# Kernel optimization log

Hardware: AMD Instinct MI355X
Metric: run time of the kernel (lower is better)

Reference implementation:

```python
import jax, jax.numpy as jnp
import numpy as np

B, NQ, NK, D = 64, 1024, 1024, 128
MASK_VALUE = -1e6


def setup_inputs() -> dict:
    key = jax.random.key(0)
    kq, kk, kv, kl = jax.random.split(key, 4)
    queries = jax.random.normal(kq, (B, NQ, D), dtype=jnp.float32)
    keys = jax.random.normal(kk, (B, NK, D), dtype=jnp.float32)
    values = jax.random.normal(kv, (B, NK, D), dtype=jnp.float32)
    valid_lens = jax.random.randint(kl, (B,), 1, NK + 1, dtype=jnp.int32)
    return {"queries": queries, "keys": keys, "values": values, "valid_lens": valid_lens}


def reference(queries, keys, values, valid_lens):
    d = queries.shape[-1]
    # scores: [B, Nq, Nk]
    scores = jnp.einsum("bqd,bkd->bqk", queries, keys) / jnp.sqrt(jnp.float32(d))
    # valid_lens [B] -> mask over last (key) axis, same for every query row
    key_pos = jnp.arange(scores.shape[-1])  # [Nk]
    mask = key_pos[None, None, :] < valid_lens[:, None, None]  # [B,1,Nk] broadcast
    scores = jnp.where(mask, scores, jnp.float32(MASK_VALUE))
    attn = jax.nn.softmax(scores, axis=-1)
    # dropout p=0.0 (eval): identity
    return jnp.einsum("bqk,bkd->bqd", attn, values)
```

## Files before the change

kernel.cpp:

```cpp
#include <hip/hip_runtime.h>

typedef __bf16 bf16x8 __attribute__((ext_vector_type(8)));
typedef __bf16 bf16x2 __attribute__((ext_vector_type(2)));
typedef float f32x4 __attribute__((ext_vector_type(4)));
typedef int i32x4 __attribute__((ext_vector_type(4)));

namespace {
constexpr int kNQ = 1024;
constexpr int kNK = 1024;
constexpr int kD = 128;
constexpr int kBQ = 64;
constexpr int kBK = 32;
constexpr int kTileElems = 4096;
constexpr float kScaleLog2e = 0.12751742f;
}

__device__ __forceinline__ int packbf(float a, float b) {
    bf16x2 t; t[0] = (__bf16)a; t[1] = (__bf16)b;
    return __builtin_bit_cast(int, t);
}

__device__ __forceinline__ void async16(const __bf16* g, const __bf16* l) {
    __builtin_amdgcn_global_load_lds(
        (const __attribute__((address_space(1))) void*)g,
        (__attribute__((address_space(3))) void*)l, 16, 0, 0);
}

__global__ void repack(const float* __restrict__ K, const float* __restrict__ V,
                       const int* __restrict__ VL,
                       __bf16* __restrict__ Kimg, __bf16* __restrict__ Vimg,
                       int* __restrict__ perm) {
    const int blk = blockIdx.x;

    if (blk == 64 * 32) {
        const int t = threadIdx.x;
        if (t < 64) {
            const int v = VL[t];
            int rank = 0;
            for (int j = 0; j < 64; ++j) {
                const int vj = VL[j];
                rank += (vj > v) || (vj == v && j < t);
            }
            perm[rank] = t;
        }
        return;
    }

    const int b = blk >> 5, t = blk & 31;
    if (t * kBK >= VL[b]) return;
    const int tid = threadIdx.x;
    __shared__ float vbuf[32 * 132];

    const size_t tileofs = (size_t)(b * 32 + t) * kTileElems;

    #pragma unroll
    for (int it = 0; it < 2; ++it) {
        const int chunk = tid + it * 256;
        const int k = chunk >> 4;
        const int p = chunk & 15;
        const int c = p ^ (k & 15);
        const float* src = K + (((size_t)b * kNK + t * kBK + k) * kD + c * 8);
        const f32x4 x0 = *(const f32x4*)src;
        const f32x4 x1 = *(const f32x4*)(src + 4);
        bf16x8 h;
        #pragma unroll
        for (int j = 0; j < 4; ++j) { h[j] = (__bf16)x0[j]; h[4 + j] = (__bf16)x1[j]; }
        *(bf16x8*)(Kimg + tileofs + chunk * 8) = h;
    }

    {
        const int r = tid >> 3, col0 = (tid & 7) * 16;
        const float* src = V + (((size_t)b * kNK + t * kBK + r) * kD + col0);
        #pragma unroll
        for (int j = 0; j < 4; ++j) {
            const f32x4 x = *(const f32x4*)(src + j * 4);
            *(f32x4*)&vbuf[r * 132 + col0 + j * 4] = x;
        }
    }
    __syncthreads();
    #pragma unroll
    for (int it = 0; it < 2; ++it) {
        const int chunk = tid + it * 256;
        const int d = chunk >> 2;
        const int p = chunk & 3;
        const int q = p ^ ((d >> 1) & 3);
        bf16x8 h;
        #pragma unroll
        for (int j = 0; j < 8; ++j) h[j] = (__bf16)vbuf[(q * 8 + j) * 132 + d];
        *(bf16x8*)(Vimg + tileofs + chunk * 8) = h;
    }
}

__global__ __launch_bounds__(256, 4)
void fa_fwd(const float* __restrict__ Q, const int* __restrict__ VL,
            const int* __restrict__ perm, const __bf16* __restrict__ Kimg,
            const __bf16* __restrict__ Vimg, float* __restrict__ O)
{
    __shared__ __align__(16) __bf16 kls[2][kTileElems];
    __shared__ __align__(16) __bf16 vls[2][kTileElems];

    const int tid  = threadIdx.x;
    const int wave = tid >> 6;
    const int lane = tid & 63;
    const int quad = lane >> 4;
    const int c16  = lane & 15;

    const int i = blockIdx.x;
    const int g = i >> 8;
    const int j = i & 255;
    int rank;
    if      (g == 0) rank = j;
    else if (g == 1) rank = 511 - j;
    else if (g == 2) rank = 512 + j;
    else             rank = 1023 - j;

    const int b    = perm[rank >> 4];
    const int qblk = rank & 15;
    const int q0   = qblk * kBQ + wave * 16;

    const int valid  = VL[b];
    const int ntiles = (valid + kBK - 1) / kBK;
    const size_t bT  = (size_t)b * 32;

    bf16x8 qf[4];
    {
        const float* qp = Q + ((size_t)b * kNQ + q0 + c16) * kD + quad * 8;
        #pragma unroll
        for (int f = 0; f < 4; ++f) {
            const f32x4 x0 = *(const f32x4*)(qp + f * 32);
            const f32x4 x1 = *(const f32x4*)(qp + f * 32 + 4);
            #pragma unroll
            for (int jj = 0; jj < 4; ++jj) {
                qf[f][jj]     = (__bf16)x0[jj];
                qf[f][4 + jj] = (__bf16)x1[jj];
            }
        }
    }

    bf16x8 ones;
    #pragma unroll
    for (int jj = 0; jj < 8; ++jj) ones[jj] = (__bf16)1.0f;

    f32x4 acc[9];
    #pragma unroll
    for (int f = 0; f < 9; ++f) {
        acc[f][0] = 0.f; acc[f][1] = 0.f; acc[f][2] = 0.f; acc[f][3] = 0.f;
    }

    auto stage = [&](int bufi, int t) {
        const __bf16* kg = Kimg + (bT + t) * kTileElems;
        const __bf16* vg = Vimg + (bT + t) * kTileElems;
        #pragma unroll
        for (int ii = 0; ii < 2; ++ii) {
            const int seg = (wave * 2 + ii) * 512;
            async16(kg + seg + lane * 8, &kls[bufi][seg]);
            async16(vg + seg + lane * 8, &vls[bufi][seg]);
        }
    };

    const int a0 = ((quad & 1) << 7) + (c16 << 2);
    const int a1 = a0 + 64;
    const bool lo = quad < 2;

    const int vsw = (quad ^ ((c16 >> 1) & 3)) << 3;

    stage(0, 0);
    __syncthreads();

    for (int t = 0; t < ntiles; ++t) {
        const int cur = t & 1;
        if (t + 1 < ntiles) stage(cur ^ 1, t + 1);

        f32x4 s0a = {0.f,0.f,0.f,0.f}, s0b = {0.f,0.f,0.f,0.f};
        f32x4 s1a = {0.f,0.f,0.f,0.f}, s1b = {0.f,0.f,0.f,0.f};
        const __bf16* kbuf = kls[cur];
        #pragma unroll
        for (int f = 0; f < 2; ++f) {
            const bf16x8 kf = *(const bf16x8*)&kbuf[c16 * 128 + (((f * 4 + quad) ^ c16) << 3)];
            s0a = __builtin_amdgcn_mfma_f32_16x16x32_bf16(kf, qf[f], s0a, 0, 0, 0);
        }
        #pragma unroll
        for (int f = 2; f < 4; ++f) {
            const bf16x8 kf = *(const bf16x8*)&kbuf[c16 * 128 + (((f * 4 + quad) ^ c16) << 3)];
            s0b = __builtin_amdgcn_mfma_f32_16x16x32_bf16(kf, qf[f], s0b, 0, 0, 0);
        }
        #pragma unroll
        for (int f = 0; f < 2; ++f) {
            const bf16x8 kf = *(const bf16x8*)&kbuf[(16 + c16) * 128 + (((f * 4 + quad) ^ c16) << 3)];
            s1a = __builtin_amdgcn_mfma_f32_16x16x32_bf16(kf, qf[f], s1a, 0, 0, 0);
        }
        #pragma unroll
        for (int f = 2; f < 4; ++f) {
            const bf16x8 kf = *(const bf16x8*)&kbuf[(16 + c16) * 128 + (((f * 4 + quad) ^ c16) << 3)];
            s1b = __builtin_amdgcn_mfma_f32_16x16x32_bf16(kf, qf[f], s1b, 0, 0, 0);
        }
        f32x4 s0 = s0a + s0b;
        f32x4 s1 = s1a + s1b;

        const int kb = t * kBK;
        if (kb + kBK > valid) {
            #pragma unroll
            for (int r = 0; r < 4; ++r) {
                if (kb + quad * 4 + r >= valid)      s0[r] = -1e30f;
                if (kb + 16 + quad * 4 + r >= valid) s1[r] = -1e30f;
            }
        }

        #pragma unroll
        for (int r = 0; r < 4; ++r) {
            s0[r] = __builtin_amdgcn_exp2f(s0[r] * kScaleLog2e);
            s1[r] = __builtin_amdgcn_exp2f(s1[r] * kScaleLog2e);
        }

        const int pp01 = packbf(s0[0], s0[1]), pp23 = packbf(s0[2], s0[3]);
        const int qq01 = packbf(s1[0], s1[1]), qq23 = packbf(s1[2], s1[3]);
        const int b0p = __builtin_amdgcn_ds_bpermute(a0, pp01);
        const int b0q = __builtin_amdgcn_ds_bpermute(a0, qq01);
        const int b1p = __builtin_amdgcn_ds_bpermute(a0, pp23);
        const int b1q = __builtin_amdgcn_ds_bpermute(a0, qq23);
        const int b2p = __builtin_amdgcn_ds_bpermute(a1, pp01);
        const int b2q = __builtin_amdgcn_ds_bpermute(a1, qq01);
        const int b3p = __builtin_amdgcn_ds_bpermute(a1, pp23);
        const int b3q = __builtin_amdgcn_ds_bpermute(a1, qq23);
        i32x4 pd;
        pd[0] = lo ? b0p : b0q;
        pd[1] = lo ? b1p : b1q;
        pd[2] = lo ? b2p : b2q;
        pd[3] = lo ? b3p : b3q;
        const bf16x8 pf = __builtin_bit_cast(bf16x8, pd);

        const __bf16* vbuf = vls[cur];
        #pragma unroll
        for (int f = 0; f < 8; ++f) {
            const bf16x8 vf = *(const bf16x8*)&vbuf[(f * 16 + c16) * 32 + vsw];
            acc[f] = __builtin_amdgcn_mfma_f32_16x16x32_bf16(pf, vf, acc[f], 0, 0, 0);
        }
        acc[8] = __builtin_amdgcn_mfma_f32_16x16x32_bf16(pf, ones, acc[8], 0, 0, 0);

        __syncthreads();
    }

    float* ob = O + ((size_t)b * kNQ + q0) * kD;
    #pragma unroll
    for (int r = 0; r < 4; ++r) {
        const float inv = 1.0f / acc[8][r];
        #pragma unroll
        for (int f = 0; f < 8; ++f) {
            ob[(quad * 4 + r) * kD + f * 16 + c16] = acc[f][r] * inv;
        }
    }
}

extern "C" void kernel_launch(void* const* d_in, const int* in_sizes, int n_in,
                              void* d_out, int out_size, void* d_ws, size_t ws_size,
                              hipStream_t stream) {
    const float* Q = (const float*)d_in[0];
    const float* K = (const float*)d_in[1];
    const float* V = (const float*)d_in[2];
    const int*  VL = (const int*)d_in[3];
    float* O = (float*)d_out;

    int* perm = (int*)d_ws;
    __bf16* Kimg = (__bf16*)((char*)d_ws + 4096);
    __bf16* Vimg = (__bf16*)((char*)d_ws + 4096 + (size_t)16 * 1024 * 1024);

    repack<<<dim3(64 * 32 + 1), 256, 0, stream>>>(K, V, VL, Kimg, Vimg, perm);
    fa_fwd<<<dim3(1024), 256, 0, stream>>>(Q, VL, perm, Kimg, Vimg, O);
}
```

Measured before the change: 165.8 us.

## Load K tiles directly into registers in MFMA fragment order, bypassing LDS

The prep kernel now writes the bf16 K image in per-lane MFMA fragment order, so each wave loads its K fragments straight from global memory into registers with coalesced 16-byte loads instead of staging through LDS. The main loop is unrolled by two with ping-pong register buffers (kA/kB) that prefetch the next tile's K while V still goes through double-buffered LDS. This halves LDS traffic and LDS footprint, which could raise occupancy. In exchange it adds 16 bf16x8 register fragments per thread, and each of the four waves re-reads the same K tile from global memory or L2.

```diff
diff --git a/kernel.cpp b/kernel.cpp
--- a/kernel.cpp
+++ b/kernel.cpp
@@ -55,17 +55,20 @@
 
     #pragma unroll
     for (int it = 0; it < 2; ++it) {
-        const int chunk = tid + it * 256;
-        const int k = chunk >> 4;
-        const int p = chunk & 15;
-        const int c = p ^ (k & 15);
-        const float* src = K + (((size_t)b * kNK + t * kBK + k) * kD + c * 8);
+        const int ch = tid + it * 256;
+        const int s  = ch >> 8;
+        const int f  = (ch >> 6) & 3;
+        const int qd = (ch >> 4) & 3;
+        const int c  = ch & 15;
+        const int key = s * 16 + c;
+        const int dch = f * 4 + qd;
+        const float* src = K + (((size_t)b * kNK + t * kBK + key) * kD + dch * 8);
         const f32x4 x0 = *(const f32x4*)src;
         const f32x4 x1 = *(const f32x4*)(src + 4);
         bf16x8 h;
         #pragma unroll
         for (int j = 0; j < 4; ++j) { h[j] = (__bf16)x0[j]; h[4 + j] = (__bf16)x1[j]; }
-        *(bf16x8*)(Kimg + tileofs + chunk * 8) = h;
+        *(bf16x8*)(Kimg + tileofs + ch * 8) = h;
     }
 
     {
@@ -96,7 +99,6 @@
             const int* __restrict__ perm, const __bf16* __restrict__ Kimg,
             const __bf16* __restrict__ Vimg, float* __restrict__ O)
 {
-    __shared__ __align__(16) __bf16 kls[2][kTileElems];
     __shared__ __align__(16) __bf16 vls[2][kTileElems];
 
     const int tid  = threadIdx.x;
@@ -122,6 +124,26 @@
     const int ntiles = (valid + kBK - 1) / kBK;
     const size_t bT  = (size_t)b * 32;
 
+    auto stage = [&](int bufi, int t) {
+        const __bf16* vg = Vimg + (bT + t) * kTileElems;
+        #pragma unroll
+        for (int ii = 0; ii < 2; ++ii) {
+            const int seg = (wave * 2 + ii) * 512;
+            async16(vg + seg + lane * 8, &vls[bufi][seg]);
+        }
+    };
+
+    bf16x8 kA[8], kB[8];
+#define LOADK(dst, tt) do {                                              \
+        const __bf16* kg_ = Kimg + (bT + (tt)) * kTileElems;             \
+        _Pragma("unroll")                                                \
+        for (int u = 0; u < 8; ++u)                                      \
+            dst[u] = *(const bf16x8*)(kg_ + u * 512 + lane * 8);         \
+    } while (0)
+
+    LOADK(kA, 0);
+    stage(0, 0);
+
     bf16x8 qf[4];
     {
         const float* qp = Q + ((size_t)b * kNQ + q0 + c16) * kD + quad * 8;
@@ -147,53 +169,23 @@
         acc[f][0] = 0.f; acc[f][1] = 0.f; acc[f][2] = 0.f; acc[f][3] = 0.f;
     }
 
-    auto stage = [&](int bufi, int t) {
-        const __bf16* kg = Kimg + (bT + t) * kTileElems;
-        const __bf16* vg = Vimg + (bT + t) * kTileElems;
-        #pragma unroll
-        for (int ii = 0; ii < 2; ++ii) {
-            const int seg = (wave * 2 + ii) * 512;
-            async16(kg + seg + lane * 8, &kls[bufi][seg]);
-            async16(vg + seg + lane * 8, &vls[bufi][seg]);
-        }
-    };
-
     const int a0 = ((quad & 1) << 7) + (c16 << 2);
     const int a1 = a0 + 64;
     const bool lo = quad < 2;
 
     const int vsw = (quad ^ ((c16 >> 1) & 3)) << 3;
 
-    stage(0, 0);
-    __syncthreads();
-
-    for (int t = 0; t < ntiles; ++t) {
-        const int cur = t & 1;
-        if (t + 1 < ntiles) stage(cur ^ 1, t + 1);
-
+    auto computeTile = [&](const bf16x8 (&kfr)[8], const __bf16* vbuf, int t) {
         f32x4 s0a = {0.f,0.f,0.f,0.f}, s0b = {0.f,0.f,0.f,0.f};
         f32x4 s1a = {0.f,0.f,0.f,0.f}, s1b = {0.f,0.f,0.f,0.f};
-        const __bf16* kbuf = kls[cur];
-        #pragma unroll
-        for (int f = 0; f < 2; ++f) {
-            const bf16x8 kf = *(const bf16x8*)&kbuf[c16 * 128 + (((f * 4 + quad) ^ c16) << 3)];
-            s0a = __builtin_amdgcn_mfma_f32_16x16x32_bf16(kf, qf[f], s0a, 0, 0, 0);
-        }
-        #pragma unroll
-        for (int f = 2; f < 4; ++f) {
-            const bf16x8 kf = *(const bf16x8*)&kbuf[c16 * 128 + (((f * 4 + quad) ^ c16) << 3)];
-            s0b = __builtin_amdgcn_mfma_f32_16x16x32_bf16(kf, qf[f], s0b, 0, 0, 0);
-        }
-        #pragma unroll
-        for (int f = 0; f < 2; ++f) {
-            const bf16x8 kf = *(const bf16x8*)&kbuf[(16 + c16) * 128 + (((f * 4 + quad) ^ c16) << 3)];
-            s1a = __builtin_amdgcn_mfma_f32_16x16x32_bf16(kf, qf[f], s1a, 0, 0, 0);
-        }
-        #pragma unroll
-        for (int f = 2; f < 4; ++f) {
-            const bf16x8 kf = *(const bf16x8*)&kbuf[(16 + c16) * 128 + (((f * 4 + quad) ^ c16) << 3)];
-            s1b = __builtin_amdgcn_mfma_f32_16x16x32_bf16(kf, qf[f], s1b, 0, 0, 0);
-        }
+        s0a = __builtin_amdgcn_mfma_f32_16x16x32_bf16(kfr[0], qf[0], s0a, 0, 0, 0);
+        s0a = __builtin_amdgcn_mfma_f32_16x16x32_bf16(kfr[1], qf[1], s0a, 0, 0, 0);
+        s0b = __builtin_amdgcn_mfma_f32_16x16x32_bf16(kfr[2], qf[2], s0b, 0, 0, 0);
+        s0b = __builtin_amdgcn_mfma_f32_16x16x32_bf16(kfr[3], qf[3], s0b, 0, 0, 0);
+        s1a = __builtin_amdgcn_mfma_f32_16x16x32_bf16(kfr[4], qf[0], s1a, 0, 0, 0);
+        s1a = __builtin_amdgcn_mfma_f32_16x16x32_bf16(kfr[5], qf[1], s1a, 0, 0, 0);
+        s1b = __builtin_amdgcn_mfma_f32_16x16x32_bf16(kfr[6], qf[2], s1b, 0, 0, 0);
+        s1b = __builtin_amdgcn_mfma_f32_16x16x32_bf16(kfr[7], qf[3], s1b, 0, 0, 0);
         f32x4 s0 = s0a + s0b;
         f32x4 s1 = s1a + s1b;
 
@@ -229,16 +221,32 @@
         pd[3] = lo ? b3p : b3q;
         const bf16x8 pf = __builtin_bit_cast(bf16x8, pd);
 
-        const __bf16* vbuf = vls[cur];
         #pragma unroll
         for (int f = 0; f < 8; ++f) {
             const bf16x8 vf = *(const bf16x8*)&vbuf[(f * 16 + c16) * 32 + vsw];
             acc[f] = __builtin_amdgcn_mfma_f32_16x16x32_bf16(pf, vf, acc[f], 0, 0, 0);
         }
         acc[8] = __builtin_amdgcn_mfma_f32_16x16x32_bf16(pf, ones, acc[8], 0, 0, 0);
-
+    };
+
+    __syncthreads();
+
+    int t = 0;
+    while (true) {
+        const bool more1 = (t + 1 < ntiles);
+        if (more1) { LOADK(kB, t + 1); stage(1, t + 1); }
+        computeTile(kA, vls[0], t);
         __syncthreads();
-    }
+        if (!more1) break;
+
+        const bool more2 = (t + 2 < ntiles);
+        if (more2) { LOADK(kA, t + 2); stage(0, t + 2); }
+        computeTile(kB, vls[1], t + 1);
+        __syncthreads();
+        if (!more2) break;
+        t += 2;
+    }
+#undef LOADK
 
     float* ob = O + ((size_t)b * kNQ + q0) * kD;
     #pragma unroll
```

Result: slower. 265.1 us (+59.9%).

## Use 512-thread blocks with 4-slot LDS ring and prefetch depth two

Applied to the files above, without the earlier changes.

Doubles the query rows per block to 128 (8 waves) so each staged K/V tile is shared by twice as many waves, halving K/V LDS traffic per query. It replaces the double buffer plus end-of-iteration __syncthreads with a 4-slot ring prefetched two tiles ahead, gated by explicit vmcnt waits and a single s_barrier. It also raises wave priority around the MFMA sections. The cost is more LDS per block (64 KB), fewer blocks to balance across CUs under variable valid lengths, and reliance on hand-written vmcnt counts being correct.

```diff
diff --git a/kernel.cpp b/kernel.cpp
--- a/kernel.cpp
+++ b/kernel.cpp
@@ -9,7 +9,6 @@
 constexpr int kNQ = 1024;
 constexpr int kNK = 1024;
 constexpr int kD = 128;
-constexpr int kBQ = 64;
 constexpr int kBK = 32;
 constexpr int kTileElems = 4096;
 constexpr float kScaleLog2e = 0.12751742f;
@@ -91,13 +90,13 @@
     }
 }
 
-__global__ __launch_bounds__(256, 4)
+__global__ __launch_bounds__(512, 4)
 void fa_fwd(const float* __restrict__ Q, const int* __restrict__ VL,
             const int* __restrict__ perm, const __bf16* __restrict__ Kimg,
             const __bf16* __restrict__ Vimg, float* __restrict__ O)
 {
-    __shared__ __align__(16) __bf16 kls[2][kTileElems];
-    __shared__ __align__(16) __bf16 vls[2][kTileElems];
+    __shared__ __align__(16) __bf16 kls[4][kTileElems];
+    __shared__ __align__(16) __bf16 vls[4][kTileElems];
 
     const int tid  = threadIdx.x;
     const int wave = tid >> 6;
@@ -106,21 +105,26 @@
     const int c16  = lane & 15;
 
     const int i = blockIdx.x;
-    const int g = i >> 8;
     const int j = i & 255;
-    int rank;
-    if      (g == 0) rank = j;
-    else if (g == 1) rank = 511 - j;
-    else if (g == 2) rank = 512 + j;
-    else             rank = 1023 - j;
-
-    const int b    = perm[rank >> 4];
-    const int qblk = rank & 15;
-    const int q0   = qblk * kBQ + wave * 16;
+    const int rank = (i >> 8) ? (511 - j) : j;
+
+    const int b  = perm[rank >> 3];
+    const int q0 = (rank & 7) * 128 + wave * 16;
 
     const int valid  = VL[b];
     const int ntiles = (valid + kBK - 1) / kBK;
     const size_t bT  = (size_t)b * 32;
+
+    auto stage = [&](int slot, int t) {
+        const __bf16* kg = Kimg + (bT + t) * kTileElems;
+        const __bf16* vg = Vimg + (bT + t) * kTileElems;
+        const int seg = wave * 512;
+        async16(kg + seg + lane * 8, &kls[slot][seg]);
+        async16(vg + seg + lane * 8, &vls[slot][seg]);
+    };
+
+    stage(0, 0);
+    if (ntiles > 1) stage(1, 1);
 
     bf16x8 qf[4];
     {
@@ -147,33 +151,30 @@
         acc[f][0] = 0.f; acc[f][1] = 0.f; acc[f][2] = 0.f; acc[f][3] = 0.f;
     }
 
-    auto stage = [&](int bufi, int t) {
-        const __bf16* kg = Kimg + (bT + t) * kTileElems;
-        const __bf16* vg = Vimg + (bT + t) * kTileElems;
-        #pragma unroll
-        for (int ii = 0; ii < 2; ++ii) {
-            const int seg = (wave * 2 + ii) * 512;
-            async16(kg + seg + lane * 8, &kls[bufi][seg]);
-            async16(vg + seg + lane * 8, &vls[bufi][seg]);
-        }
-    };
-
     const int a0 = ((quad & 1) << 7) + (c16 << 2);
     const int a1 = a0 + 64;
     const bool lo = quad < 2;
 
     const int vsw = (quad ^ ((c16 >> 1) & 3)) << 3;
 
-    stage(0, 0);
-    __syncthreads();
-
     for (int t = 0; t < ntiles; ++t) {
-        const int cur = t & 1;
-        if (t + 1 < ntiles) stage(cur ^ 1, t + 1);
+        if (t + 2 < ntiles) {
+            stage((t + 2) & 3, t + 2);
+            asm volatile("s_waitcnt vmcnt(4)" ::: "memory");
+        } else if (t + 1 < ntiles) {
+            asm volatile("s_waitcnt vmcnt(2)" ::: "memory");
+        } else {
+            asm volatile("s_waitcnt vmcnt(0)" ::: "memory");
+        }
+        __builtin_amdgcn_s_barrier();
+        __builtin_amdgcn_sched_barrier(0);
+
+        const __bf16* kbuf = kls[t & 3];
+        const __bf16* vbuf = vls[t & 3];
 
         f32x4 s0a = {0.f,0.f,0.f,0.f}, s0b = {0.f,0.f,0.f,0.f};
         f32x4 s1a = {0.f,0.f,0.f,0.f}, s1b = {0.f,0.f,0.f,0.f};
-        const __bf16* kbuf = kls[cur];
+        __builtin_amdgcn_s_setprio(1);
         #pragma unroll
         for (int f = 0; f < 2; ++f) {
             const bf16x8 kf = *(const bf16x8*)&kbuf[c16 * 128 + (((f * 4 + quad) ^ c16) << 3)];
@@ -194,6 +195,7 @@
             const bf16x8 kf = *(const bf16x8*)&kbuf[(16 + c16) * 128 + (((f * 4 + quad) ^ c16) << 3)];
             s1b = __builtin_amdgcn_mfma_f32_16x16x32_bf16(kf, qf[f], s1b, 0, 0, 0);
         }
+        __builtin_amdgcn_s_setprio(0);
         f32x4 s0 = s0a + s0b;
         f32x4 s1 = s1a + s1b;
 
@@ -229,15 +231,14 @@
         pd[3] = lo ? b3p : b3q;
         const bf16x8 pf = __builtin_bit_cast(bf16x8, pd);
 
-        const __bf16* vbuf = vls[cur];
+        __builtin_amdgcn_s_setprio(1);
+        acc[8] = __builtin_amdgcn_mfma_f32_16x16x32_bf16(pf, ones, acc[8], 0, 0, 0);
         #pragma unroll
         for (int f = 0; f < 8; ++f) {
             const bf16x8 vf = *(const bf16x8*)&vbuf[(f * 16 + c16) * 32 + vsw];
             acc[f] = __builtin_amdgcn_mfma_f32_16x16x32_bf16(pf, vf, acc[f], 0, 0, 0);
         }
-        acc[8] = __builtin_amdgcn_mfma_f32_16x16x32_bf16(pf, ones, acc[8], 0, 0, 0);
-
-        __syncthreads();
+        __builtin_amdgcn_s_setprio(0);
     }
 
     float* ob = O + ((size_t)b * kNQ + q0) * kD;
@@ -265,5 +266,5 @@
     __bf16* Vimg = (__bf16*)((char*)d_ws + 4096 + (size_t)16 * 1024 * 1024);
 
     repack<<<dim3(64 * 32 + 1), 256, 0, stream>>>(K, V, VL, Kimg, Vimg, perm);
-    fa_fwd<<<dim3(1024), 256, 0, stream>>>(Q, VL, perm, Kimg, Vimg, O);
-}
+    fa_fwd<<<dim3(512), 512, 0, stream>>>(Q, VL, perm, Kimg, Vimg, O);
+}
```

New measurement: 164.1 us. Within noise of the previous version (-1.0%).
